# Kernel tuning notes

Hardware: AMD Instinct MI355X
Metric: run time of the kernel (lower is better)

## Reference

```python
import jax, jax.numpy as jnp
import numpy as np

N_NODES = 65536
N_GRAPHS = 1024
NODES_PER_G = 64
N_EDGES = 1048576
IN_FEATS = 512
HIDDEN = 1024
H4 = 256
EMB = 512
EPS = 1e-5
SLOPE = 0.01


def setup_inputs() -> dict:
    key = jax.random.key(0)
    ks = jax.random.split(key, 10)
    # within-graph random edges: edge e belongs to graph e // (E/B)
    epg = N_EDGES // N_GRAPHS
    eg = np.arange(N_EDGES) // epg
    rng = np.random.default_rng(0)
    src = rng.integers(0, NODES_PER_G, N_EDGES) + eg * NODES_PER_G
    dst = rng.integers(0, NODES_PER_G, N_EDGES) + eg * NODES_PER_G
    node_gid = np.arange(N_NODES) // NODES_PER_G
    return {
        "node_feats": jax.random.normal(ks[0], (N_NODES, IN_FEATS), jnp.float32),
        "edge_weights": jax.random.uniform(ks[1], (N_EDGES,), jnp.float32),
        "W1": jax.random.normal(ks[2], (IN_FEATS, HIDDEN), jnp.float32) * 0.05,
        "W2": jax.random.normal(ks[3], (HIDDEN, H4), jnp.float32) * 0.05,
        "W_emb": jax.random.normal(ks[4], (IN_FEATS + HIDDEN + H4, EMB), jnp.float32) * 0.02,
        "gn1_alpha": jnp.ones((HIDDEN,), jnp.float32),
        "gn1_gamma": jnp.ones((HIDDEN,), jnp.float32),
        "gn1_beta": jnp.zeros((HIDDEN,), jnp.float32),
        "gn2_alpha": jnp.ones((H4,), jnp.float32),
        "gn2_gamma": jnp.ones((H4,), jnp.float32),
        "gn2_beta": jnp.zeros((H4,), jnp.float32),
        "edge_src": jnp.asarray(src, jnp.int32),
        "edge_dst": jnp.asarray(dst, jnp.int32),
        "node_gid": jnp.asarray(node_gid, jnp.int32),
    }


def _seg_sum(x, ids, num):
    return jax.ops.segment_sum(x, ids, num_segments=num)


def _graph_conv(x, W, src, dst, ew):
    # DGL GraphConv, norm='both', bias=False, with edge_weight (u_mul_e)
    ones = jnp.ones((src.shape[0],), x.dtype)
    deg_out = jnp.clip(_seg_sum(ones, src, N_NODES), 1.0)
    deg_in = jnp.clip(_seg_sum(ones, dst, N_NODES), 1.0)
    h = (x * jax.lax.rsqrt(deg_out)[:, None]) @ W
    msg = h[src] * ew[:, None]
    agg = _seg_sum(msg, dst, N_NODES)
    return agg * jax.lax.rsqrt(deg_in)[:, None]


def _graph_norm(x, gid, counts, alpha, gamma, beta):
    # GraphNorm (Cai et al.): learnable mean-scale alpha, per-graph stats
    mean = _seg_sum(x, gid, N_GRAPHS) / counts[:, None]
    sub = x - alpha * mean[gid]
    var = _seg_sum(sub * sub, gid, N_GRAPHS) / counts[:, None]
    return gamma * sub * jax.lax.rsqrt(var[gid] + EPS) + beta


def _mean_nodes(x, gid, counts):
    return _seg_sum(x, gid, N_GRAPHS) / counts[:, None]


def _leaky(x):
    return jnp.where(x >= 0, x, SLOPE * x)


def reference(node_feats, edge_weights, W1, W2, W_emb,
              gn1_alpha, gn1_gamma, gn1_beta,
              gn2_alpha, gn2_gamma, gn2_beta,
              edge_src, edge_dst, node_gid):
    counts = jnp.clip(_seg_sum(jnp.ones((N_NODES,), node_feats.dtype), node_gid, N_GRAPHS), 1.0)
    r0 = _mean_nodes(node_feats, node_gid, counts)                 # [B, in]
    h1 = _graph_conv(node_feats, W1, edge_src, edge_dst, edge_weights)
    h1 = _leaky(_graph_norm(h1, node_gid, counts, gn1_alpha, gn1_gamma, gn1_beta))
    r1 = _mean_nodes(h1, node_gid, counts)                          # [B, hidden]
    h2 = _graph_conv(h1, W2, edge_src, edge_dst, edge_weights)
    h2 = _leaky(_graph_norm(h2, node_gid, counts, gn2_alpha, gn2_gamma, gn2_beta))
    r2 = _mean_nodes(h2, node_gid, counts)                          # [B, hidden/4]
    emb = jnp.concatenate([r0, r1, r2], axis=1) @ W_emb             # [B, EMB]
    # InstanceNorm1d on [B, E] input: per-row normalization, no affine
    mu = jnp.mean(emb, axis=1, keepdims=True)
    var = jnp.mean((emb - mu) ** 2, axis=1, keepdims=True)
    emb = (emb - mu) * jax.lax.rsqrt(var + EPS)
    return _leaky(emb)
```

## Files before the change

kernel.cpp:

```cpp
#include <hip/hip_runtime.h>
#include <hip/hip_bf16.h>
#include <stdint.h>

#define N_NODES   65536
#define N_GRAPHS  1024
#define N_EDGES   1048576
#define IN_FEATS  512
#define HIDDEN    1024
#define H4        256
#define EMB_DIM   512
#define RDIM      1792
#define EPS_F     1e-5f
#define SLOPE_F   0.01f

typedef __bf16 bf16;
typedef __bf16 bf16x8 __attribute__((ext_vector_type(8)));
typedef float  floatx4 __attribute__((ext_vector_type(4)));

#define GLDS16(gp, lp) __builtin_amdgcn_global_load_lds( \
    (const __attribute__((address_space(1))) void*)(gp), \
    (__attribute__((address_space(3))) void*)(lp), 16, 0, 0)

__global__ __launch_bounds__(256) void k_graph_build(
    const int* __restrict__ src, const int* __restrict__ dst,
    const float* __restrict__ ew,
    bf16* __restrict__ adjb, float* __restrict__ scl_o)
{
    __shared__ float sAdj[4096];
    __shared__ float sDegO[64], sDegI[64];
    int g = blockIdx.x, tid = threadIdx.x;
    for (int i = tid; i < 4096; i += 256) sAdj[i] = 0.f;
    if (tid < 64) { sDegO[tid] = 0.f; sDegI[tid] = 0.f; }
    __syncthreads();
    int e0 = g * 1024;
    #pragma unroll
    for (int i = 0; i < 4; ++i) {
        int e = e0 + i * 256 + tid;
        int s = src[e] & 63, d = dst[e] & 63;
        atomicAdd(&sAdj[(d << 6) | s], ew[e]);
        atomicAdd(&sDegO[s], 1.f);
        atomicAdd(&sDegI[d], 1.f);
    }
    __syncthreads();
    if (tid < 64) scl_o[g * 64 + tid] = rsqrtf(fmaxf(sDegO[tid], 1.f));
    bf16* ag = adjb + ((size_t)g << 12);
    for (int i = tid; i < 4096; i += 256) {
        float si = rsqrtf(fmaxf(sDegI[i >> 6], 1.f));
        ag[i] = (bf16)(sAdj[i] * si);
    }
}

__global__ __launch_bounds__(256) void k_transpose(
    const float* __restrict__ W, bf16* __restrict__ WT, int K, int logN)
{
    int idx = blockIdx.x * 256 + threadIdx.x;
    if (idx >= (K << logN)) return;
    int n = idx & ((1 << logN) - 1);
    int k = idx >> logN;
    WT[(size_t)n * K + k] = (bf16)W[idx];
}

__global__ __launch_bounds__(256) void k_prep_agg1(
    const float* __restrict__ x, const float* __restrict__ so,
    const bf16* __restrict__ adjb,
    bf16* __restrict__ axs1, bf16* __restrict__ Rb)
{
    __shared__ __align__(16) bf16 sOut[64 * 264];
    __shared__ float sSo[64];
    int g = blockIdx.x >> 1, half = blockIdx.x & 1;
    int tid = threadIdx.x, lane = tid & 63, wave = tid >> 6, q = lane >> 4;
    if (tid < 64) sSo[tid] = so[g * 64 + tid];
    const float* xg = x + (size_t)g * 64 * IN_FEATS + half * 256;
    const bf16* ag = adjb + ((size_t)g << 12);

    bf16x8 af[4][2];
    #pragma unroll
    for (int mt = 0; mt < 4; ++mt)
        #pragma unroll
        for (int kk = 0; kk < 2; ++kk)
            af[mt][kk] = *(const bf16x8*)&ag[(mt * 16 + (lane & 15)) * 64 + kk * 32 + q * 8];
    __syncthreads();
    float sov[2][8];
    #pragma unroll
    for (int kk = 0; kk < 2; ++kk)
        #pragma unroll
        for (int j = 0; j < 8; ++j) sov[kk][j] = sSo[kk * 32 + q * 8 + j];

    #pragma unroll
    for (int nt = 0; nt < 4; ++nt) {
        int cl = wave * 64 + nt * 16 + (lane & 15);
        floatx4 acc[4] = {};
        float r0 = 0.f;
        #pragma unroll
        for (int kk = 0; kk < 2; ++kk) {
            bf16x8 bfrag;
            #pragma unroll
            for (int j = 0; j < 8; ++j) {
                float v = xg[(size_t)(kk * 32 + q * 8 + j) * IN_FEATS + cl];
                r0 += v;
                bfrag[j] = (bf16)(v * sov[kk][j]);
            }
            #pragma unroll
            for (int mt = 0; mt < 4; ++mt)
                acc[mt] = __builtin_amdgcn_mfma_f32_16x16x32_bf16(af[mt][kk], bfrag, acc[mt], 0, 0, 0);
        }
        r0 += __shfl_xor(r0, 16);
        r0 += __shfl_xor(r0, 32);
        if (lane < 16) Rb[(size_t)g * RDIM + half * 256 + cl] = (bf16)(r0 * (1.f / 64.f));
        #pragma unroll
        for (int mt = 0; mt < 4; ++mt)
            #pragma unroll
            for (int i = 0; i < 4; ++i)
                sOut[(mt * 16 + q * 4 + i) * 264 + cl] = (bf16)acc[mt][i];
    }
    __syncthreads();
    #pragma unroll
    for (int it = 0; it < 8; ++it) {
        int idx = it * 256 + tid;
        int d = idx >> 5, c8 = idx & 31;
        *(bf16x8*)&axs1[(size_t)(g * 64 + d) * IN_FEATS + half * 256 + c8 * 8] =
            *(const bf16x8*)&sOut[d * 264 + c8 * 8];
    }
}

__global__ __launch_bounds__(512) void k_gemm12(
    const bf16* __restrict__ A, const bf16* __restrict__ BT1,
    const bf16* __restrict__ BT2, const bf16* __restrict__ adjb,
    const float* __restrict__ al1, const float* __restrict__ ga1, const float* __restrict__ be1,
    const float* __restrict__ al2, const float* __restrict__ ga2, const float* __restrict__ be2,
    const float* __restrict__ so, bf16* __restrict__ Rb)
{
    __shared__ __align__(16) bf16 sm[66560];
    __shared__ float sSo[128];
    const int tid = threadIdx.x;
    const int lane = tid & 63, wave = tid >> 6, q = lane >> 4;
    const int wm = wave >> 2, wn = wave & 3;
    const int by = blockIdx.x;
    const int row0 = by * 128;
    const int gw = by * 2 + wm;
    if (tid < 128) sSo[tid] = so[row0 + tid];

    floatx4 acc2[4][4] = {};
    bf16* sX = sm + 49152;

    #pragma unroll 1
    for (int ct = 0; ct < 8; ++ct) {
        floatx4 acc1[4][2] = {};

        auto stage_ab = [&](int k0, int buf) {
            #pragma unroll
            for (int ro = 0; ro < 2; ++ro) {
                int u = ro * 4096 + wave * 512 + lane * 8;
                int r = u >> 6, c = ((u >> 3) & 7) ^ (r & 7);
                GLDS16(A   + (size_t)(row0 + r) * IN_FEATS + k0 + c * 8,
                       sm + buf * 16384 + ro * 4096 + wave * 512);
                GLDS16(BT1 + (size_t)(ct * 128 + r) * IN_FEATS + k0 + c * 8,
                       sm + buf * 16384 + 8192 + ro * 4096 + wave * 512);
            }
        };
        auto stage_w2 = [&](int h, int buf) {
            #pragma unroll
            for (int ro = 0; ro < 4; ++ro) {
                int u = ro * 4096 + wave * 512 + lane * 8;
                int r = u >> 6, c = ((u >> 3) & 7) ^ (r & 7);
                GLDS16(BT2 + (size_t)r * HIDDEN + ct * 128 + h * 64 + c * 8,
                       sm + buf * 16384 + ro * 4096 + wave * 512);
            }
        };
        auto mfma_step = [&](int buf) {
            const bf16* sA = sm + buf * 16384;
            const bf16* sB = sA + 8192;
            #pragma unroll
            for (int kk = 0; kk < 2; ++kk) {
                bf16x8 afr[4], bfr[2];
                int cw = kk * 4 + q;
                #pragma unroll
                for (int mt = 0; mt < 4; ++mt) {
                    int r = wm * 64 + mt * 16 + (lane & 15);
                    afr[mt] = *(const bf16x8*)&sA[(r * 8 + (cw ^ (r & 7))) * 8];
                }
                #pragma unroll
                for (int nt = 0; nt < 2; ++nt) {
                    int r = wn * 32 + nt * 16 + (lane & 15);
                    bfr[nt] = *(const bf16x8*)&sB[(r * 8 + (cw ^ (r & 7))) * 8];
                }
                #pragma unroll
                for (int mt = 0; mt < 4; ++mt)
                    #pragma unroll
                    for (int nt = 0; nt < 2; ++nt)
                        acc1[mt][nt] = __builtin_amdgcn_mfma_f32_16x16x32_bf16(
                            afr[mt], bfr[nt], acc1[mt][nt], 0, 0, 0);
            }
        };

        stage_ab(0, 0);
        stage_ab(64, 1);

        #pragma unroll
        for (int t = 0; t < 8; ++t) {
            asm volatile("s_waitcnt vmcnt(4)" ::: "memory");
            __builtin_amdgcn_s_barrier();
            if (t < 6)       stage_ab((t + 2) * 64, (t + 2) % 3);
            else if (t == 6) stage_w2(0, 2);
            else             stage_w2(1, 0);
            mfma_step(t % 3);
        }

        #pragma unroll
        for (int nt = 0; nt < 2; ++nt) {
            int cl = wn * 32 + nt * 16 + (lane & 15);
            int colg = ct * 128 + cl;
            float lsum = 0.f;
            #pragma unroll
            for (int mt = 0; mt < 4; ++mt)
                #pragma unroll
                for (int i = 0; i < 4; ++i) lsum += acc1[mt][nt][i];
            lsum += __shfl_xor(lsum, 16);
            lsum += __shfl_xor(lsum, 32);
            float am = al1[colg] * (lsum * (1.f / 64.f));
            float gm = ga1[colg], bt = be1[colg];
            float sub[4][4], qv = 0.f;
            #pragma unroll
            for (int mt = 0; mt < 4; ++mt)
                #pragma unroll
                for (int i = 0; i < 4; ++i) {
                    float d = acc1[mt][nt][i] - am;
                    sub[mt][i] = d; qv += d * d;
                }
            qv += __shfl_xor(qv, 16);
            qv += __shfl_xor(qv, 32);
            float rs = rsqrtf(qv * (1.f / 64.f) + EPS_F);
            float rsum = 0.f;
            #pragma unroll
            for (int mt = 0; mt < 4; ++mt)
                #pragma unroll
                for (int i = 0; i < 4; ++i) {
                    float o = gm * sub[mt][i] * rs + bt;
                    o = (o >= 0.f) ? o : SLOPE_F * o;
                    rsum += o;
                    int r = wm * 64 + mt * 16 + q * 4 + i;
                    sX[r * 136 + cl] = (bf16)(o * sSo[r]);
                }
            rsum += __shfl_xor(rsum, 16);
            rsum += __shfl_xor(rsum, 32);
            if (lane < 16)
                Rb[(size_t)gw * RDIM + 512 + colg] = (bf16)(rsum * (1.f / 64.f));
        }
        asm volatile("s_waitcnt vmcnt(0)" ::: "memory");
        __syncthreads();

        #pragma unroll
        for (int kk2 = 0; kk2 < 4; ++kk2) {
            const bf16* sW = sm + ((kk2 < 2) ? 2 : 0) * 16384;
            int cw = (kk2 & 1) * 4 + q;
            bf16x8 afr[4], bfr[4];
            #pragma unroll
            for (int mt = 0; mt < 4; ++mt)
                afr[mt] = *(const bf16x8*)&sX[(wm * 64 + mt * 16 + (lane & 15)) * 136 + kk2 * 32 + q * 8];
            #pragma unroll
            for (int nt = 0; nt < 4; ++nt) {
                int r = wn * 64 + nt * 16 + (lane & 15);
                bfr[nt] = *(const bf16x8*)&sW[(r * 8 + (cw ^ (r & 7))) * 8];
            }
            #pragma unroll
            for (int mt = 0; mt < 4; ++mt)
                #pragma unroll
                for (int nt = 0; nt < 4; ++nt)
                    acc2[mt][nt] = __builtin_amdgcn_mfma_f32_16x16x32_bf16(
                        afr[mt], bfr[nt], acc2[mt][nt], 0, 0, 0);
        }
        __syncthreads();
    }

    bf16* sT = sm;
    #pragma unroll
    for (int nt = 0; nt < 4; ++nt) {
        int cl = wn * 64 + nt * 16 + (lane & 15);
        #pragma unroll
        for (int mt = 0; mt < 4; ++mt)
            #pragma unroll
            for (int i = 0; i < 4; ++i)
                sT[cl * 136 + wm * 64 + mt * 16 + q * 4 + i] = (bf16)acc2[mt][nt][i];
    }
    asm volatile("s_waitcnt lgkmcnt(0)" ::: "memory");

    const bf16* ag = adjb + ((size_t)gw << 12);
    floatx4 hh[4][4] = {};
    #pragma unroll
    for (int kk = 0; kk < 2; ++kk) {
        bf16x8 afr[4], bfr[4];
        #pragma unroll
        for (int mt = 0; mt < 4; ++mt)
            afr[mt] = *(const bf16x8*)&ag[(mt * 16 + (lane & 15)) * 64 + kk * 32 + q * 8];
        #pragma unroll
        for (int nt = 0; nt < 4; ++nt)
            bfr[nt] = *(const bf16x8*)&sT[(wn * 64 + nt * 16 + (lane & 15)) * 136 + wm * 64 + kk * 32 + q * 8];
        #pragma unroll
        for (int mt = 0; mt < 4; ++mt)
            #pragma unroll
            for (int nt = 0; nt < 4; ++nt)
                hh[mt][nt] = __builtin_amdgcn_mfma_f32_16x16x32_bf16(afr[mt], bfr[nt], hh[mt][nt], 0, 0, 0);
    }

    #pragma unroll
    for (int nt = 0; nt < 4; ++nt) {
        int colg = wn * 64 + nt * 16 + (lane & 15);
        float lsum = 0.f;
        #pragma unroll
        for (int mt = 0; mt < 4; ++mt)
            #pragma unroll
            for (int i = 0; i < 4; ++i) lsum += hh[mt][nt][i];
        lsum += __shfl_xor(lsum, 16);
        lsum += __shfl_xor(lsum, 32);
        float am = al2[colg] * (lsum * (1.f / 64.f));
        float gm = ga2[colg], bt = be2[colg];
        float sub[4][4], qv = 0.f;
        #pragma unroll
        for (int mt = 0; mt < 4; ++mt)
            #pragma unroll
            for (int i = 0; i < 4; ++i) {
                float d = hh[mt][nt][i] - am;
                sub[mt][i] = d; qv += d * d;
            }
        qv += __shfl_xor(qv, 16);
        qv += __shfl_xor(qv, 32);
        float rs = rsqrtf(qv * (1.f / 64.f) + EPS_F);
        float rsum = 0.f;
        #pragma unroll
        for (int mt = 0; mt < 4; ++mt)
            #pragma unroll
            for (int i = 0; i < 4; ++i) {
                float o = gm * sub[mt][i] * rs + bt;
                rsum += (o >= 0.f) ? o : SLOPE_F * o;
            }
        rsum += __shfl_xor(rsum, 16);
        rsum += __shfl_xor(rsum, 32);
        if (lane < 16)
            Rb[(size_t)gw * RDIM + 1536 + colg] = (bf16)(rsum * (1.f / 64.f));
    }
}

__device__ __forceinline__ void gemm_mainloop_db(
    const bf16* __restrict__ A, const bf16* __restrict__ BT, int K,
    int row0, int col0, int lane, int wave, int wm, int wn, int q,
    bf16* sm, floatx4 (&acc)[4][4])
{
    auto stage = [&](int k0, int buf) {
        #pragma unroll
        for (int i = 0; i < 4; ++i) {
            int u = (wave * 4 + i) * 64 + lane;
            int r = u >> 3, c = (u & 7) ^ (r & 7);
            GLDS16(A  + (size_t)(row0 + r) * K + (k0 + c * 8),
                   sm + buf * 16384 + (wave * 4 + i) * 512);
            GLDS16(BT + (size_t)(col0 + r) * K + (k0 + c * 8),
                   sm + buf * 16384 + 8192 + (wave * 4 + i) * 512);
        }
    };
    auto step = [&](int buf) {
        const bf16* sA = sm + buf * 16384;
        const bf16* sB = sA + 8192;
        #pragma unroll
        for (int kk = 0; kk < 2; ++kk) {
            bf16x8 afr[4], bfr[4];
            int cw = kk * 4 + q;
            #pragma unroll
            for (int mt = 0; mt < 4; ++mt) {
                int r = wm * 64 + mt * 16 + (lane & 15);
                afr[mt] = *(const bf16x8*)&sA[(r * 8 + (cw ^ (r & 7))) * 8];
            }
            #pragma unroll
            for (int nt = 0; nt < 4; ++nt) {
                int r = wn * 64 + nt * 16 + (lane & 15);
                bfr[nt] = *(const bf16x8*)&sB[(r * 8 + (cw ^ (r & 7))) * 8];
            }
            #pragma unroll
            for (int mt = 0; mt < 4; ++mt)
                #pragma unroll
                for (int nt = 0; nt < 4; ++nt)
                    acc[mt][nt] = __builtin_amdgcn_mfma_f32_16x16x32_bf16(
                        afr[mt], bfr[nt], acc[mt][nt], 0, 0, 0);
        }
    };
    stage(0, 0);
    asm volatile("s_waitcnt vmcnt(0)" ::: "memory");
    __syncthreads();
    int cur = 0;
    const int nsteps = K >> 6;
    #pragma unroll 1
    for (int t = 0; t < nsteps - 1; ++t) {
        stage((t + 1) << 6, cur ^ 1);
        step(cur);
        asm volatile("s_waitcnt vmcnt(0)" ::: "memory");
        __syncthreads();
        cur ^= 1;
    }
    step(cur);
}

__device__ __forceinline__ void swizzle_block(int cb, int& bx, int& by)
{
    int b = blockIdx.y * gridDim.x + blockIdx.x;
    int xcd = b & 7, t = b >> 3;
    bx = t % cb;
    by = (t / cb) * 8 + xcd;
}

__global__ __launch_bounds__(256) void k_gemm_ro(
    const bf16* __restrict__ A, const bf16* __restrict__ BT,
    float* __restrict__ Cout)
{
    __shared__ __align__(16) bf16 sm[32768];
    const int tid = threadIdx.x;
    const int lane = tid & 63, wave = tid >> 6, q = lane >> 4;
    const int wm = wave & 1, wn = wave >> 1;
    int bx, by; swizzle_block(gridDim.x, bx, by);
    const int row0 = by * 128, col0 = bx * 128;

    floatx4 acc[4][4] = {};
    gemm_mainloop_db(A, BT, RDIM, row0, col0, lane, wave, wm, wn, q, sm, acc);

    #pragma unroll
    for (int mt = 0; mt < 4; ++mt)
        #pragma unroll
        for (int nt = 0; nt < 4; ++nt) {
            int col = col0 + wn * 64 + nt * 16 + (lane & 15);
            #pragma unroll
            for (int i = 0; i < 4; ++i) {
                int row = row0 + wm * 64 + mt * 16 + q * 4 + i;
                Cout[(size_t)row * EMB_DIM + col] = acc[mt][nt][i];
            }
        }
}

__global__ __launch_bounds__(256) void k_instnorm(
    const float* __restrict__ emb, float* __restrict__ out)
{
    int row = blockIdx.x, tid = threadIdx.x;
    int lane = tid & 63, wave = tid >> 6;
    __shared__ float sS[4], sQ[4];
    float v0 = emb[(size_t)row * EMB_DIM + tid];
    float v1 = emb[(size_t)row * EMB_DIM + 256 + tid];
    float s = v0 + v1, q = v0 * v0 + v1 * v1;
    #pragma unroll
    for (int off = 32; off; off >>= 1) {
        s += __shfl_down(s, off);
        q += __shfl_down(q, off);
    }
    if (lane == 0) { sS[wave] = s; sQ[wave] = q; }
    __syncthreads();
    float S = sS[0] + sS[1] + sS[2] + sS[3];
    float Q = sQ[0] + sQ[1] + sQ[2] + sQ[3];
    float mu = S * (1.f / 512.f);
    float var = Q * (1.f / 512.f) - mu * mu;
    float rs = rsqrtf(var + EPS_F);
    float o0 = (v0 - mu) * rs; o0 = (o0 >= 0.f) ? o0 : SLOPE_F * o0;
    float o1 = (v1 - mu) * rs; o1 = (o1 >= 0.f) ? o1 : SLOPE_F * o1;
    out[(size_t)row * EMB_DIM + tid]       = o0;
    out[(size_t)row * EMB_DIM + 256 + tid] = o1;
}

extern "C" void kernel_launch(void* const* d_in, const int* in_sizes, int n_in,
                              void* d_out, int out_size, void* d_ws, size_t ws_size,
                              hipStream_t stream) {
    const float* x    = (const float*)d_in[0];
    const float* ew   = (const float*)d_in[1];
    const float* W1   = (const float*)d_in[2];
    const float* W2   = (const float*)d_in[3];
    const float* Wemb = (const float*)d_in[4];
    const float* a1   = (const float*)d_in[5];
    const float* g1   = (const float*)d_in[6];
    const float* b1   = (const float*)d_in[7];
    const float* a2   = (const float*)d_in[8];
    const float* g2   = (const float*)d_in[9];
    const float* b2   = (const float*)d_in[10];
    const int* esrc   = (const int*)d_in[11];
    const int* edst   = (const int*)d_in[12];
    float* out = (float*)d_out;

    char* ws = (char*)d_ws;
    const size_t MB = 1024ull * 1024ull;
    bf16*  adjb   = (bf16*)(ws);
    float* scl_o  = (float*)(ws + 8 * MB);
    bf16*  Rb     = (bf16*)(ws + 9 * MB);
    bf16*  W1T    = (bf16*)(ws + 13 * MB);
    bf16*  W2T    = (bf16*)(ws + 14 * MB);
    bf16*  WembT  = (bf16*)(ws + 15 * MB);
    float* emb    = (float*)(ws + 17 * MB);
    bf16*  axs1   = (bf16*)(ws + 20 * MB);

    k_graph_build<<<N_GRAPHS, 256, 0, stream>>>(esrc, edst, ew, adjb, scl_o);
    k_transpose<<<2048, 256, 0, stream>>>(W1, W1T, 512, 10);
    k_transpose<<<1024, 256, 0, stream>>>(W2, W2T, 1024, 8);
    k_transpose<<<3584, 256, 0, stream>>>(Wemb, WembT, 1792, 9);

    k_prep_agg1<<<N_GRAPHS * 2, 256, 0, stream>>>(x, scl_o, adjb, axs1, Rb);

    k_gemm12<<<N_NODES / 128, 512, 0, stream>>>(
        axs1, W1T, W2T, adjb, a1, g1, b1, a2, g2, b2, scl_o, Rb);

    k_gemm_ro<<<dim3(EMB_DIM / 128, N_GRAPHS / 128), 256, 0, stream>>>(
        Rb, WembT, emb);
    k_instnorm<<<N_GRAPHS, 256, 0, stream>>>(emb, out);

    (void)in_sizes; (void)n_in; (void)out_size; (void)ws_size;
}
```

Measured before the change: 437.0 us.

## Coalesce prep_agg1 input loads via LDS and quad-buffer the readout GEMM

In k_prep_agg1, each wave now reads node features with coalesced float4 row loads, applies the out-degree scale, and stores bf16 into LDS. The graph-mean readout is reduced through LDS, and MFMA B fragments come from LDS instead of strided scalar global loads. The readout GEMM k_gemm_ro drops the double-buffered helper for an inlined four-stage pipeline keeping three tiles in flight, using vmcnt waits and raw s_barrier. This doubles LDS use to 128KB per block and hardcodes the K loop count, which can lower occupancy and depends on exact vmcnt accounting for correctness.

```diff
diff --git a/kernel.cpp b/kernel.cpp
--- a/kernel.cpp
+++ b/kernel.cpp
@@ -14,6 +14,7 @@
 #define SLOPE_F   0.01f
 
 typedef __bf16 bf16;
+typedef __bf16 bf16x4 __attribute__((ext_vector_type(4)));
 typedef __bf16 bf16x8 __attribute__((ext_vector_type(8)));
 typedef float  floatx4 __attribute__((ext_vector_type(4)));
 
@@ -65,11 +66,15 @@
     const bf16* __restrict__ adjb,
     bf16* __restrict__ axs1, bf16* __restrict__ Rb)
 {
+    __shared__ __align__(16) bf16 sXr[64 * 260];
     __shared__ __align__(16) bf16 sOut[64 * 264];
+    __shared__ float sR[4][256];
     __shared__ float sSo[64];
     int g = blockIdx.x >> 1, half = blockIdx.x & 1;
     int tid = threadIdx.x, lane = tid & 63, wave = tid >> 6, q = lane >> 4;
     if (tid < 64) sSo[tid] = so[g * 64 + tid];
+    __syncthreads();
+
     const float* xg = x + (size_t)g * 64 * IN_FEATS + half * 256;
     const bf16* ag = adjb + ((size_t)g << 12);
 
@@ -79,34 +84,44 @@
         #pragma unroll
         for (int kk = 0; kk < 2; ++kk)
             af[mt][kk] = *(const bf16x8*)&ag[(mt * 16 + (lane & 15)) * 64 + kk * 32 + q * 8];
+
+    float r0a = 0.f, r0b = 0.f, r0c = 0.f, r0d = 0.f;
+    #pragma unroll
+    for (int i = 0; i < 16; ++i) {
+        int row = i * 4 + wave;
+        float4 v = *(const float4*)&xg[(size_t)row * IN_FEATS + lane * 4];
+        r0a += v.x; r0b += v.y; r0c += v.z; r0d += v.w;
+        float sc = sSo[row];
+        bf16x4 p;
+        p[0] = (bf16)(v.x * sc); p[1] = (bf16)(v.y * sc);
+        p[2] = (bf16)(v.z * sc); p[3] = (bf16)(v.w * sc);
+        *(bf16x4*)&sXr[row * 260 + lane * 4] = p;
+    }
+    sR[wave][lane * 4 + 0] = r0a;
+    sR[wave][lane * 4 + 1] = r0b;
+    sR[wave][lane * 4 + 2] = r0c;
+    sR[wave][lane * 4 + 3] = r0d;
     __syncthreads();
-    float sov[2][8];
-    #pragma unroll
-    for (int kk = 0; kk < 2; ++kk)
-        #pragma unroll
-        for (int j = 0; j < 8; ++j) sov[kk][j] = sSo[kk * 32 + q * 8 + j];
+
+    {
+        float s = sR[0][tid] + sR[1][tid] + sR[2][tid] + sR[3][tid];
+        Rb[(size_t)g * RDIM + half * 256 + tid] = (bf16)(s * (1.f / 64.f));
+    }
 
     #pragma unroll
     for (int nt = 0; nt < 4; ++nt) {
         int cl = wave * 64 + nt * 16 + (lane & 15);
         floatx4 acc[4] = {};
-        float r0 = 0.f;
         #pragma unroll
         for (int kk = 0; kk < 2; ++kk) {
             bf16x8 bfrag;
             #pragma unroll
-            for (int j = 0; j < 8; ++j) {
-                float v = xg[(size_t)(kk * 32 + q * 8 + j) * IN_FEATS + cl];
-                r0 += v;
-                bfrag[j] = (bf16)(v * sov[kk][j]);
-            }
+            for (int j = 0; j < 8; ++j)
+                bfrag[j] = sXr[(kk * 32 + q * 8 + j) * 260 + cl];
             #pragma unroll
             for (int mt = 0; mt < 4; ++mt)
                 acc[mt] = __builtin_amdgcn_mfma_f32_16x16x32_bf16(af[mt][kk], bfrag, acc[mt], 0, 0, 0);
         }
-        r0 += __shfl_xor(r0, 16);
-        r0 += __shfl_xor(r0, 32);
-        if (lane < 16) Rb[(size_t)g * RDIM + half * 256 + cl] = (bf16)(r0 * (1.f / 64.f));
         #pragma unroll
         for (int mt = 0; mt < 4; ++mt)
             #pragma unroll
@@ -340,63 +355,6 @@
     }
 }
 
-__device__ __forceinline__ void gemm_mainloop_db(
-    const bf16* __restrict__ A, const bf16* __restrict__ BT, int K,
-    int row0, int col0, int lane, int wave, int wm, int wn, int q,
-    bf16* sm, floatx4 (&acc)[4][4])
-{
-    auto stage = [&](int k0, int buf) {
-        #pragma unroll
-        for (int i = 0; i < 4; ++i) {
-            int u = (wave * 4 + i) * 64 + lane;
-            int r = u >> 3, c = (u & 7) ^ (r & 7);
-            GLDS16(A  + (size_t)(row0 + r) * K + (k0 + c * 8),
-                   sm + buf * 16384 + (wave * 4 + i) * 512);
-            GLDS16(BT + (size_t)(col0 + r) * K + (k0 + c * 8),
-                   sm + buf * 16384 + 8192 + (wave * 4 + i) * 512);
-        }
-    };
-    auto step = [&](int buf) {
-        const bf16* sA = sm + buf * 16384;
-        const bf16* sB = sA + 8192;
-        #pragma unroll
-        for (int kk = 0; kk < 2; ++kk) {
-            bf16x8 afr[4], bfr[4];
-            int cw = kk * 4 + q;
-            #pragma unroll
-            for (int mt = 0; mt < 4; ++mt) {
-                int r = wm * 64 + mt * 16 + (lane & 15);
-                afr[mt] = *(const bf16x8*)&sA[(r * 8 + (cw ^ (r & 7))) * 8];
-            }
-            #pragma unroll
-            for (int nt = 0; nt < 4; ++nt) {
-                int r = wn * 64 + nt * 16 + (lane & 15);
-                bfr[nt] = *(const bf16x8*)&sB[(r * 8 + (cw ^ (r & 7))) * 8];
-            }
-            #pragma unroll
-            for (int mt = 0; mt < 4; ++mt)
-                #pragma unroll
-                for (int nt = 0; nt < 4; ++nt)
-                    acc[mt][nt] = __builtin_amdgcn_mfma_f32_16x16x32_bf16(
-                        afr[mt], bfr[nt], acc[mt][nt], 0, 0, 0);
-        }
-    };
-    stage(0, 0);
-    asm volatile("s_waitcnt vmcnt(0)" ::: "memory");
-    __syncthreads();
-    int cur = 0;
-    const int nsteps = K >> 6;
-    #pragma unroll 1
-    for (int t = 0; t < nsteps - 1; ++t) {
-        stage((t + 1) << 6, cur ^ 1);
-        step(cur);
-        asm volatile("s_waitcnt vmcnt(0)" ::: "memory");
-        __syncthreads();
-        cur ^= 1;
-    }
-    step(cur);
-}
-
 __device__ __forceinline__ void swizzle_block(int cb, int& bx, int& by)
 {
     int b = blockIdx.y * gridDim.x + blockIdx.x;
@@ -409,7 +367,7 @@
     const bf16* __restrict__ A, const bf16* __restrict__ BT,
     float* __restrict__ Cout)
 {
-    __shared__ __align__(16) bf16 sm[32768];
+    __shared__ __align__(16) bf16 sm[65536];
     const int tid = threadIdx.x;
     const int lane = tid & 63, wave = tid >> 6, q = lane >> 4;
     const int wm = wave & 1, wn = wave >> 1;
@@ -417,7 +375,58 @@
     const int row0 = by * 128, col0 = bx * 128;
 
     floatx4 acc[4][4] = {};
-    gemm_mainloop_db(A, BT, RDIM, row0, col0, lane, wave, wm, wn, q, sm, acc);
+
+    auto stage = [&](int k0, int buf) {
+        #pragma unroll
+        for (int i = 0; i < 4; ++i) {
+            int u = (wave * 4 + i) * 64 + lane;
+            int r = u >> 3, c = (u & 7) ^ (r & 7);
+            GLDS16(A  + (size_t)(row0 + r) * RDIM + (k0 + c * 8),
+                   sm + buf * 16384 + (wave * 4 + i) * 512);
+            GLDS16(BT + (size_t)(col0 + r) * RDIM + (k0 + c * 8),
+                   sm + buf * 16384 + 8192 + (wave * 4 + i) * 512);
+        }
+    };
+    auto step = [&](int buf) {
+        const bf16* sA = sm + buf * 16384;
+        const bf16* sB = sA + 8192;
+        #pragma unroll
+        for (int kk = 0; kk < 2; ++kk) {
+            bf16x8 afr[4], bfr[4];
+            int cw = kk * 4 + q;
+            #pragma unroll
+            for (int mt = 0; mt < 4; ++mt) {
+                int r = wm * 64 + mt * 16 + (lane & 15);
+                afr[mt] = *(const bf16x8*)&sA[(r * 8 + (cw ^ (r & 7))) * 8];
+            }
+            #pragma unroll
+            for (int nt = 0; nt < 4; ++nt) {
+                int r = wn * 64 + nt * 16 + (lane & 15);
+                bfr[nt] = *(const bf16x8*)&sB[(r * 8 + (cw ^ (r & 7))) * 8];
+            }
+            #pragma unroll
+            for (int mt = 0; mt < 4; ++mt)
+                #pragma unroll
+                for (int nt = 0; nt < 4; ++nt)
+                    acc[mt][nt] = __builtin_amdgcn_mfma_f32_16x16x32_bf16(
+                        afr[mt], bfr[nt], acc[mt][nt], 0, 0, 0);
+        }
+    };
+
+    stage(0, 0); stage(64, 1); stage(128, 2);
+    #pragma unroll 1
+    for (int t = 0; t < 26; ++t) {
+        asm volatile("s_waitcnt vmcnt(16)" ::: "memory");
+        __builtin_amdgcn_s_barrier();
+        if (t < 25) stage((t + 3) * 64, (t + 3) & 3);
+        step(t & 3);
+    }
+    asm volatile("s_waitcnt vmcnt(8)" ::: "memory");
+    __builtin_amdgcn_s_barrier();
+    step(2);
+    asm volatile("s_waitcnt vmcnt(0)" ::: "memory");
+    __builtin_amdgcn_s_barrier();
+    step(3);
 
     #pragma unroll
     for (int mt = 0; mt < 4; ++mt)
```

Result: faster. 424.0 us (-3.0%).
